# Optimization experiments

Measured on AMD Instinct MI355X. Metric: run time of the kernel, lower is better.

Reference implementation:

```python
import jax, jax.numpy as jnp
import numpy as np

N_NODES = 50000
N_EDGES = 320000
D_IN = 256
D_OUT = 256


def setup_inputs() -> dict:
    key = jax.random.key(0)
    k1, k2, k3, k4, k5, k6, k7 = jax.random.split(key, 7)
    s = 1.0 / np.sqrt(D_IN)
    return {
        "node_features": jax.random.normal(k1, (N_NODES, D_IN), dtype=jnp.float32),
        "edge_index": jax.random.randint(k2, (2, N_EDGES), 0, N_NODES, dtype=jnp.int64),
        "w1": jax.random.uniform(k3, (D_OUT, D_IN), jnp.float32, -s, s),
        "w2": jax.random.uniform(k4, (D_OUT, D_IN), jnp.float32, -s, s),
        "w3": jax.random.uniform(k5, (D_OUT, D_IN), jnp.float32, -s, s),
        "b3": jax.random.uniform(k6, (D_OUT,), jnp.float32, -s, s),
    }


def reference(node_features, edge_index, w1, w2, w3, b3):
    # GraphSAGE-style conv: project, gather messages from senders,
    # scatter-sum at receivers, project, combine with self term.
    n = node_features.shape[0]
    proj = node_features @ w3.T + b3                 # [N, D_OUT]
    msgs = proj[edge_index[0]]                       # [E, D_OUT] gather senders
    agg = jax.ops.segment_sum(msgs, edge_index[1], num_segments=n)  # [N, D_OUT]
    out = node_features @ w1.T + agg @ w2.T          # [N, D_OUT]
    return out
```

## Files before the change

### kernel.cpp

```cpp
#include <hip/hip_runtime.h>

#define NN 50000
#define NPAD 50048
#define NE 320000
#define D 256
#define CAP 64
#define NCONV 6250

typedef __bf16 bf16x8 __attribute__((ext_vector_type(8)));
typedef float f32x4 __attribute__((ext_vector_type(4)));

__device__ __forceinline__ unsigned short f2bf(float f) {
    unsigned u = __builtin_bit_cast(unsigned, f);
    unsigned r = u + 0x7FFFu + ((u >> 16) & 1u);
    return (unsigned short)(r >> 16);
}
__device__ __forceinline__ float bflo(unsigned u) {
    return __builtin_bit_cast(float, u << 16);
}
__device__ __forceinline__ float bfhi(unsigned u) {
    return __builtin_bit_cast(float, u & 0xFFFF0000u);
}
__device__ __forceinline__ unsigned packbf(float lo, float hi) {
    return (unsigned)f2bf(lo) | ((unsigned)f2bf(hi) << 16);
}

__global__ __launch_bounds__(256) void prep_weights(
        const float* __restrict__ w1, const float* __restrict__ w2,
        const float* __restrict__ w3, const float* __restrict__ b3,
        unsigned short* __restrict__ WTT, float* __restrict__ bvec,
        int* __restrict__ cnt) {
    const int j = blockIdx.x;
    const int k = threadIdx.x;
    const int g = j * 256 + k;
    if (g < NN) cnt[g] = 0;
    __shared__ float w2row[D];
    __shared__ float red[D];
    w2row[k] = w2[j * D + k];
    __syncthreads();
    float acc = 0.f;
    #pragma unroll 8
    for (int o = 0; o < D; ++o) acc += w2row[o] * w3[o * D + k];
    WTT[(size_t)j * 512 + k]     = f2bf(w1[j * D + k]);
    WTT[(size_t)j * 512 + D + k] = f2bf(acc);
    red[k] = w2row[k] * b3[k];
    __syncthreads();
    for (int s = 128; s > 0; s >>= 1) {
        if (k < s) red[k] += red[k + s];
        __syncthreads();
    }
    if (k == 0) bvec[j] = red[0];
}

__global__ __launch_bounds__(256) void convert_and_csr(
        const float* __restrict__ x, unsigned short* __restrict__ xbf,
        const int* __restrict__ ei, int* __restrict__ csr, int* __restrict__ cnt) {
    const int b = blockIdx.x;
    if (b < NCONV) {
        const size_t i = ((size_t)b * 256 + threadIdx.x) * 8;
        const float4 a0 = *reinterpret_cast<const float4*>(x + i);
        const float4 a1 = *reinterpret_cast<const float4*>(x + i + 4);
        ushort4 o0 = {f2bf(a0.x), f2bf(a0.y), f2bf(a0.z), f2bf(a0.w)};
        ushort4 o1 = {f2bf(a1.x), f2bf(a1.y), f2bf(a1.z), f2bf(a1.w)};
        *reinterpret_cast<ushort4*>(xbf + i)     = o0;
        *reinterpret_cast<ushort4*>(xbf + i + 4) = o1;
    } else {
        const int e = (b - NCONV) * 256 + threadIdx.x;
        if (e < NE) {
            const int src = ei[e];
            const int dst = ei[NE + e];
            const int pos = atomicAdd(cnt + dst, 1);
            if (pos < CAP) csr[(size_t)dst * CAP + pos] = src;
        }
    }
}

__global__ __launch_bounds__(256) void agg_gather(
        const unsigned short* __restrict__ xbf, const int* __restrict__ csr,
        const int* __restrict__ cnt, unsigned short* __restrict__ aggbf) {
    const int node = blockIdx.x * 8 + (threadIdx.x >> 5);
    const int l32  = threadIdx.x & 31;
    if (node >= NN) return;
    int d = cnt[node]; if (d > CAP) d = CAP;
    const int* __restrict__ row = csr + (size_t)node * CAP;
    const int d32 = d < 32 ? d : 32;
    int myidx = 0;
    if (l32 < d32) myidx = row[l32];
    float a0 = 0.f, a1 = 0.f, a2 = 0.f, a3 = 0.f;
    float a4 = 0.f, a5 = 0.f, a6 = 0.f, a7 = 0.f;
    int i = 0;
    for (; i + 4 <= d32; i += 4) {
        const int s0 = __shfl(myidx, i,     32);
        const int s1 = __shfl(myidx, i + 1, 32);
        const int s2 = __shfl(myidx, i + 2, 32);
        const int s3 = __shfl(myidx, i + 3, 32);
        const uint4 p = *reinterpret_cast<const uint4*>(xbf + (size_t)s0 * D + l32 * 8);
        const uint4 q = *reinterpret_cast<const uint4*>(xbf + (size_t)s1 * D + l32 * 8);
        const uint4 u = *reinterpret_cast<const uint4*>(xbf + (size_t)s2 * D + l32 * 8);
        const uint4 v = *reinterpret_cast<const uint4*>(xbf + (size_t)s3 * D + l32 * 8);
        a0 += (bflo(p.x) + bflo(q.x)) + (bflo(u.x) + bflo(v.x));
        a1 += (bfhi(p.x) + bfhi(q.x)) + (bfhi(u.x) + bfhi(v.x));
        a2 += (bflo(p.y) + bflo(q.y)) + (bflo(u.y) + bflo(v.y));
        a3 += (bfhi(p.y) + bfhi(q.y)) + (bfhi(u.y) + bfhi(v.y));
        a4 += (bflo(p.z) + bflo(q.z)) + (bflo(u.z) + bflo(v.z));
        a5 += (bfhi(p.z) + bfhi(q.z)) + (bfhi(u.z) + bfhi(v.z));
        a6 += (bflo(p.w) + bflo(q.w)) + (bflo(u.w) + bflo(v.w));
        a7 += (bfhi(p.w) + bfhi(q.w)) + (bfhi(u.w) + bfhi(v.w));
    }
    for (; i < d32; ++i) {
        const int s = __shfl(myidx, i, 32);
        const uint4 p = *reinterpret_cast<const uint4*>(xbf + (size_t)s * D + l32 * 8);
        a0 += bflo(p.x); a1 += bfhi(p.x);
        a2 += bflo(p.y); a3 += bfhi(p.y);
        a4 += bflo(p.z); a5 += bfhi(p.z);
        a6 += bflo(p.w); a7 += bfhi(p.w);
    }
    for (; i < d; ++i) {
        const uint4 p = *reinterpret_cast<const uint4*>(xbf + (size_t)row[i] * D + l32 * 8);
        a0 += bflo(p.x); a1 += bfhi(p.x);
        a2 += bflo(p.y); a3 += bfhi(p.y);
        a4 += bflo(p.z); a5 += bfhi(p.z);
        a6 += bflo(p.w); a7 += bfhi(p.w);
    }
    uint4 o = {packbf(a0, a1), packbf(a2, a3), packbf(a4, a5), packbf(a6, a7)};
    *reinterpret_cast<uint4*>(aggbf + (size_t)node * D + l32 * 8) = o;
}

__global__ __launch_bounds__(256) void gemm_tiled(
        const unsigned short* __restrict__ xbf, const unsigned short* __restrict__ aggbf,
        const unsigned short* __restrict__ WTT, const float* __restrict__ bvec,
        const int* __restrict__ cnt, float* __restrict__ out) {
    __shared__ __align__(16) unsigned short ldsA[64 * 64];
    __shared__ __align__(16) unsigned short ldsB[128 * 64];

    const int tid  = threadIdx.x;
    const int w    = tid >> 6;
    const int lane = tid & 63;
    const int l16  = lane & 15;
    const int g4   = lane >> 4;
    const int wm   = w >> 1, wn = w & 1;
    const int gr0  = (blockIdx.x >> 1) * 64;
    const int nb0  = (blockIdx.x & 1) * 128;

    f32x4 acc[2][4];
    #pragma unroll
    for (int a = 0; a < 2; ++a)
        #pragma unroll
        for (int b = 0; b < 4; ++b) acc[a][b] = (f32x4)0.f;

    for (int kt = 0; kt < 8; ++kt) {
        if (kt) __syncthreads();
        {
            const unsigned short* __restrict__ srcA = (kt < 4) ? xbf : aggbf;
            const int kcA = (kt & 3) * 64;
            #pragma unroll
            for (int p = 0; p < 2; ++p) {
                const int idx = p * 256 + w * 64 + lane;
                const int r = idx >> 3, c = idx & 7;
                const int sw = (c ^ (r & 7)) << 3;
                const unsigned short* gp = srcA + ((size_t)(gr0 + r) << 8) + kcA + sw;
                unsigned short* lp = &ldsA[(p * 256 + w * 64) << 3];
                __builtin_amdgcn_global_load_lds(
                    (const __attribute__((address_space(1))) void*)(const void*)gp,
                    (__attribute__((address_space(3))) void*)(void*)lp, 16, 0, 0);
            }
            const int kcB = kt * 64;
            #pragma unroll
            for (int p = 0; p < 4; ++p) {
                const int idx = p * 256 + w * 64 + lane;
                const int r = idx >> 3, c = idx & 7;
                const int sw = (c ^ (r & 7)) << 3;
                const unsigned short* gp = WTT + ((size_t)(nb0 + r) << 9) + kcB + sw;
                unsigned short* lp = &ldsB[(p * 256 + w * 64) << 3];
                __builtin_amdgcn_global_load_lds(
                    (const __attribute__((address_space(1))) void*)(const void*)gp,
                    (__attribute__((address_space(3))) void*)(void*)lp, 16, 0, 0);
            }
        }
        __syncthreads();

        #pragma unroll
        for (int kh = 0; kh < 2; ++kh) {
            const int cb = kh * 4 + g4;
            bf16x8 af[2], bfr[4];
            #pragma unroll
            for (int f = 0; f < 2; ++f) {
                const int ra = wm * 32 + f * 16 + l16;
                af[f] = *reinterpret_cast<const bf16x8*>(
                    &ldsA[(ra * 8 + (cb ^ (ra & 7))) * 8]);
            }
            #pragma unroll
            for (int f = 0; f < 4; ++f) {
                const int rb = wn * 64 + f * 16 + l16;
                bfr[f] = *reinterpret_cast<const bf16x8*>(
                    &ldsB[(rb * 8 + (cb ^ (rb & 7))) * 8]);
            }
            #pragma unroll
            for (int fm = 0; fm < 2; ++fm)
                #pragma unroll
                for (int fn = 0; fn < 4; ++fn)
                    acc[fm][fn] = __builtin_amdgcn_mfma_f32_16x16x32_bf16(
                        af[fm], bfr[fn], acc[fm][fn], 0, 0, 0);
        }
    }

    const int col0 = nb0 + wn * 64 + l16;
    float bv[4];
    #pragma unroll
    for (int fn = 0; fn < 4; ++fn) bv[fn] = bvec[col0 + fn * 16];
    #pragma unroll
    for (int fm = 0; fm < 2; ++fm) {
        #pragma unroll
        for (int i = 0; i < 4; ++i) {
            const int row = gr0 + wm * 32 + fm * 16 + g4 * 4 + i;
            if (row < NN) {
                const float dg = (float)cnt[row];
                float* op = out + ((size_t)row << 8) + col0;
                #pragma unroll
                for (int fn = 0; fn < 4; ++fn)
                    op[fn * 16] = acc[fm][fn][i] + dg * bv[fn];
            }
        }
    }
}

extern "C" void kernel_launch(void* const* d_in, const int* in_sizes, int n_in,
                              void* d_out, int out_size, void* d_ws, size_t ws_size,
                              hipStream_t stream) {
    const float* x  = (const float*)d_in[0];
    const int*   ei = (const int*)d_in[1];
    const float* w1 = (const float*)d_in[2];
    const float* w2 = (const float*)d_in[3];
    const float* w3 = (const float*)d_in[4];
    const float* b3 = (const float*)d_in[5];
    float* out = (float*)d_out;

    unsigned short* xbf   = (unsigned short*)d_ws;
    unsigned short* aggbf = xbf + (size_t)NPAD * D;
    unsigned short* WTT   = aggbf + (size_t)NPAD * D;
    float* bvec = (float*)(WTT + (size_t)D * 512);
    int*   cnt  = (int*)(bvec + D);
    int*   csr  = cnt + NN;

    prep_weights<<<D, 256, 0, stream>>>(w1, w2, w3, b3, WTT, bvec, cnt);
    convert_and_csr<<<NCONV + (NE + 255) / 256, 256, 0, stream>>>(x, xbf, ei, csr, cnt);
    agg_gather<<<(NN + 7) / 8, 256, 0, stream>>>(xbf, csr, cnt, aggbf);
    gemm_tiled<<<(NPAD / 64) * 2, 256, 0, stream>>>(xbf, aggbf, WTT, bvec, cnt, out);
}
```

Before: 101.1 us.

## Double-buffer GEMM LDS tiles with async prefetch and schedule CSR blocks first

The GEMM main loop now uses two LDS buffers per operand. It prefetches tile kt+2 while computing tile kt, with explicit vmcnt waits and barriers, so global-to-LDS loads overlap with MFMA work. The intent is to hide load latency that the previous load-sync-compute loop exposed. The convert/CSR kernel also reorders its blocks so the atomic CSR-building blocks launch before the conversion blocks, letting the atomic tail overlap with the streaming conversion. LDS use doubles, which may reduce occupancy, and the hand-written vmcnt counts must match the number of loads per stage.

```diff
diff --git a/kernel.cpp b/kernel.cpp
--- a/kernel.cpp
+++ b/kernel.cpp
@@ -5,6 +5,7 @@
 #define NE 320000
 #define D 256
 #define CAP 64
+#define NCSR 1250
 #define NCONV 6250
 
 typedef __bf16 bf16x8 __attribute__((ext_vector_type(8)));
@@ -56,22 +57,22 @@
         const float* __restrict__ x, unsigned short* __restrict__ xbf,
         const int* __restrict__ ei, int* __restrict__ csr, int* __restrict__ cnt) {
     const int b = blockIdx.x;
-    if (b < NCONV) {
-        const size_t i = ((size_t)b * 256 + threadIdx.x) * 8;
+    if (b < NCSR) {
+        const int e = b * 256 + threadIdx.x;
+        if (e < NE) {
+            const int src = ei[e];
+            const int dst = ei[NE + e];
+            const int pos = atomicAdd(cnt + dst, 1);
+            if (pos < CAP) csr[(size_t)dst * CAP + pos] = src;
+        }
+    } else {
+        const size_t i = ((size_t)(b - NCSR) * 256 + threadIdx.x) * 8;
         const float4 a0 = *reinterpret_cast<const float4*>(x + i);
         const float4 a1 = *reinterpret_cast<const float4*>(x + i + 4);
         ushort4 o0 = {f2bf(a0.x), f2bf(a0.y), f2bf(a0.z), f2bf(a0.w)};
         ushort4 o1 = {f2bf(a1.x), f2bf(a1.y), f2bf(a1.z), f2bf(a1.w)};
         *reinterpret_cast<ushort4*>(xbf + i)     = o0;
         *reinterpret_cast<ushort4*>(xbf + i + 4) = o1;
-    } else {
-        const int e = (b - NCONV) * 256 + threadIdx.x;
-        if (e < NE) {
-            const int src = ei[e];
-            const int dst = ei[NE + e];
-            const int pos = atomicAdd(cnt + dst, 1);
-            if (pos < CAP) csr[(size_t)dst * CAP + pos] = src;
-        }
     }
 }
 
@@ -130,8 +131,8 @@
         const unsigned short* __restrict__ xbf, const unsigned short* __restrict__ aggbf,
         const unsigned short* __restrict__ WTT, const float* __restrict__ bvec,
         const int* __restrict__ cnt, float* __restrict__ out) {
-    __shared__ __align__(16) unsigned short ldsA[64 * 64];
-    __shared__ __align__(16) unsigned short ldsB[128 * 64];
+    __shared__ __align__(16) unsigned short ldsA[2][64 * 64];
+    __shared__ __align__(16) unsigned short ldsB[2][128 * 64];
 
     const int tid  = threadIdx.x;
     const int w    = tid >> 6;
@@ -142,42 +143,48 @@
     const int gr0  = (blockIdx.x >> 1) * 64;
     const int nb0  = (blockIdx.x & 1) * 128;
 
+    auto stage = [&](int kt, int b) {
+        const unsigned short* __restrict__ srcA = (kt < 4) ? xbf : aggbf;
+        const int kcA = (kt & 3) * 64;
+        #pragma unroll
+        for (int p = 0; p < 2; ++p) {
+            const int idx = p * 256 + w * 64 + lane;
+            const int r = idx >> 3, c = idx & 7;
+            const int sw = (c ^ (r & 7)) << 3;
+            const unsigned short* gp = srcA + ((size_t)(gr0 + r) << 8) + kcA + sw;
+            unsigned short* lp = &ldsA[b][(p * 256 + w * 64) << 3];
+            __builtin_amdgcn_global_load_lds(
+                (const __attribute__((address_space(1))) void*)(const void*)gp,
+                (__attribute__((address_space(3))) void*)(void*)lp, 16, 0, 0);
+        }
+        const int kcB = kt * 64;
+        #pragma unroll
+        for (int p = 0; p < 4; ++p) {
+            const int idx = p * 256 + w * 64 + lane;
+            const int r = idx >> 3, c = idx & 7;
+            const int sw = (c ^ (r & 7)) << 3;
+            const unsigned short* gp = WTT + ((size_t)(nb0 + r) << 9) + kcB + sw;
+            unsigned short* lp = &ldsB[b][(p * 256 + w * 64) << 3];
+            __builtin_amdgcn_global_load_lds(
+                (const __attribute__((address_space(1))) void*)(const void*)gp,
+                (__attribute__((address_space(3))) void*)(void*)lp, 16, 0, 0);
+        }
+    };
+
     f32x4 acc[2][4];
     #pragma unroll
     for (int a = 0; a < 2; ++a)
         #pragma unroll
         for (int b = 0; b < 4; ++b) acc[a][b] = (f32x4)0.f;
 
+    stage(0, 0);
+    stage(1, 1);
+    #pragma unroll
     for (int kt = 0; kt < 8; ++kt) {
-        if (kt) __syncthreads();
-        {
-            const unsigned short* __restrict__ srcA = (kt < 4) ? xbf : aggbf;
-            const int kcA = (kt & 3) * 64;
-            #pragma unroll
-            for (int p = 0; p < 2; ++p) {
-                const int idx = p * 256 + w * 64 + lane;
-                const int r = idx >> 3, c = idx & 7;
-                const int sw = (c ^ (r & 7)) << 3;
-                const unsigned short* gp = srcA + ((size_t)(gr0 + r) << 8) + kcA + sw;
-                unsigned short* lp = &ldsA[(p * 256 + w * 64) << 3];
-                __builtin_amdgcn_global_load_lds(
-                    (const __attribute__((address_space(1))) void*)(const void*)gp,
-                    (__attribute__((address_space(3))) void*)(void*)lp, 16, 0, 0);
-            }
-            const int kcB = kt * 64;
-            #pragma unroll
-            for (int p = 0; p < 4; ++p) {
-                const int idx = p * 256 + w * 64 + lane;
-                const int r = idx >> 3, c = idx & 7;
-                const int sw = (c ^ (r & 7)) << 3;
-                const unsigned short* gp = WTT + ((size_t)(nb0 + r) << 9) + kcB + sw;
-                unsigned short* lp = &ldsB[(p * 256 + w * 64) << 3];
-                __builtin_amdgcn_global_load_lds(
-                    (const __attribute__((address_space(1))) void*)(const void*)gp,
-                    (__attribute__((address_space(3))) void*)(void*)lp, 16, 0, 0);
-            }
-        }
-        __syncthreads();
+        const int cur = kt & 1;
+        if (kt < 7) asm volatile("s_waitcnt vmcnt(6)" ::: "memory");
+        else        asm volatile("s_waitcnt vmcnt(0)" ::: "memory");
+        __builtin_amdgcn_s_barrier();
 
         #pragma unroll
         for (int kh = 0; kh < 2; ++kh) {
@@ -187,13 +194,13 @@
             for (int f = 0; f < 2; ++f) {
                 const int ra = wm * 32 + f * 16 + l16;
                 af[f] = *reinterpret_cast<const bf16x8*>(
-                    &ldsA[(ra * 8 + (cb ^ (ra & 7))) * 8]);
+                    &ldsA[cur][(ra * 8 + (cb ^ (ra & 7))) * 8]);
             }
             #pragma unroll
             for (int f = 0; f < 4; ++f) {
                 const int rb = wn * 64 + f * 16 + l16;
                 bfr[f] = *reinterpret_cast<const bf16x8*>(
-                    &ldsB[(rb * 8 + (cb ^ (rb & 7))) * 8]);
+                    &ldsB[cur][(rb * 8 + (cb ^ (rb & 7))) * 8]);
             }
             #pragma unroll
             for (int fm = 0; fm < 2; ++fm)
@@ -202,6 +209,8 @@
                     acc[fm][fn] = __builtin_amdgcn_mfma_f32_16x16x32_bf16(
                         af[fm], bfr[fn], acc[fm][fn], 0, 0, 0);
         }
+        __builtin_amdgcn_s_barrier();
+        if (kt < 6) stage(kt + 2, cur);
     }
 
     const int col0 = nb0 + wn * 64 + l16;
@@ -243,7 +252,7 @@
     int*   csr  = cnt + NN;
 
     prep_weights<<<D, 256, 0, stream>>>(w1, w2, w3, b3, WTT, bvec, cnt);
-    convert_and_csr<<<NCONV + (NE + 255) / 256, 256, 0, stream>>>(x, xbf, ei, csr, cnt);
+    convert_and_csr<<<NCSR + NCONV, 256, 0, stream>>>(x, xbf, ei, csr, cnt);
     agg_gather<<<(NN + 7) / 8, 256, 0, stream>>>(xbf, csr, cnt, aggbf);
     gemm_tiled<<<(NPAD / 64) * 2, 256, 0, stream>>>(xbf, aggbf, WTT, bvec, cnt, out);
 }
```

After: 102.8 us. No clear change (+1.6%).
